# Optimization experiments

Measured on AMD Instinct MI355X. Metric: run time of the kernel, lower is better.

The kernel has to match this reference:

```python
import jax, jax.numpy as jnp
import numpy as np
from jax import lax

B, C, H, W = 1, 512, 64, 64
HEADS, GROUPS, STRIDE, KK = 8, 4, 2, 5
HC = C // HEADS          # 64 head channels
CG = C // GROUPS         # 128 group channels
GH = HEADS // GROUPS     # 2 heads per group
OFR = 2.0                # offset_range_factor
SCALE = HC ** -0.5


def ref_points(Hk, Wk):
    # torch linspace(0.5, Hk-0.5, Hk)/Hk*2-1 == (arange+0.5)/Hk*2-1
    ry = (jnp.arange(Hk, dtype=jnp.float32) + 0.5) / Hk * 2.0 - 1.0
    rx = (jnp.arange(Wk, dtype=jnp.float32) + 0.5) / Wk * 2.0 - 1.0
    return jnp.stack(jnp.meshgrid(ry, rx, indexing='ij'), axis=-1)  # [Hk,Wk,2] (y,x)


def _gather(img, ix, iy, Hi, Wi):
    # img [N,Cc,Hi,Wi]; ix,iy float index maps [N,...]; zero padding outside
    N, Cc = img.shape[0], img.shape[1]
    valid = ((ix >= 0) & (ix <= Wi - 1) & (iy >= 0) & (iy <= Hi - 1)).astype(img.dtype)
    ixc = jnp.clip(ix, 0, Wi - 1).astype(jnp.int32)
    iyc = jnp.clip(iy, 0, Hi - 1).astype(jnp.int32)
    idx = (iyc * Wi + ixc).reshape(N, -1)
    imgf = img.reshape(N, Cc, Hi * Wi)
    g = jax.vmap(lambda im, ii: im[:, ii])(imgf, idx).reshape((N, Cc) + ix.shape[1:])
    return g * valid[:, None]


def grid_sample(img, grid):
    # bilinear, align_corners=True, zeros padding; grid [...,(x,y)] in [-1,1]
    N, Cc, Hi, Wi = img.shape
    gx = (grid[..., 0] + 1.0) * 0.5 * (Wi - 1)
    gy = (grid[..., 1] + 1.0) * 0.5 * (Hi - 1)
    x0 = jnp.floor(gx); y0 = jnp.floor(gy)
    wx = gx - x0; wy = gy - y0
    w00 = ((1 - wx) * (1 - wy))[:, None]; w01 = (wx * (1 - wy))[:, None]
    w10 = ((1 - wx) * wy)[:, None]; w11 = (wx * wy)[:, None]
    return (_gather(img, x0, y0, Hi, Wi) * w00 + _gather(img, x0 + 1, y0, Hi, Wi) * w01
            + _gather(img, x0, y0 + 1, Hi, Wi) * w10 + _gather(img, x0 + 1, y0 + 1, Hi, Wi) * w11)


def conv1x1(w, b, x):  # x [B,C,H,W]
    return jnp.einsum('oc,bchw->bohw', w, x) + b[None, :, None, None]


def setup_inputs() -> dict:
    key = jax.random.key(0)
    ks = jax.random.split(key, 8)
    d = {}
    d['x'] = jax.random.normal(ks[0], (B, C, H, W), jnp.float32)
    d['wq'] = jax.random.normal(ks[1], (C, C), jnp.float32) * 0.04
    d['bq'] = jnp.zeros((C,), jnp.float32)
    d['wk'] = jax.random.normal(ks[2], (C, C), jnp.float32) * 0.04
    d['bk'] = jnp.zeros((C,), jnp.float32)
    d['wv'] = jax.random.normal(ks[3], (C, C), jnp.float32) * 0.04
    d['bv'] = jnp.zeros((C,), jnp.float32)
    d['wo'] = jax.random.normal(ks[4], (C, C), jnp.float32) * 0.04
    d['bo'] = jnp.zeros((C,), jnp.float32)
    d['w_off_dw'] = jax.random.normal(ks[5], (CG, 1, KK, KK), jnp.float32) * 0.1
    d['b_off_dw'] = jnp.zeros((CG,), jnp.float32)
    d['ln_g'] = jnp.ones((CG,), jnp.float32)
    d['ln_b'] = jnp.zeros((CG,), jnp.float32)
    d['w_off_pw'] = jax.random.normal(ks[6], (2, CG), jnp.float32) * 0.05
    d['rpe_table'] = jax.random.normal(ks[7], (HEADS, 2 * H - 1, 2 * W - 1), jnp.float32) * 0.01
    return d


def reference(x, wq, bq, wk, bk, wv, bv, wo, bo, w_off_dw, b_off_dw, ln_g, ln_b, w_off_pw, rpe_table):
    q = conv1x1(wq, bq, x)                                   # [B,C,H,W]
    q_off = q.reshape(B * GROUPS, CG, H, W)
    # conv_offset: depthwise 5x5 stride-2 -> LayerNorm(channels) -> GELU -> 1x1 to 2ch
    t = lax.conv_general_dilated(q_off, w_off_dw, (STRIDE, STRIDE),
                                 ((KK // 2, KK // 2), (KK // 2, KK // 2)),
                                 feature_group_count=CG,
                                 dimension_numbers=('NCHW', 'OIHW', 'NCHW'))
    t = t + b_off_dw[None, :, None, None]
    mu = t.mean(1, keepdims=True)
    var = ((t - mu) ** 2).mean(1, keepdims=True)
    t = (t - mu) * lax.rsqrt(var + 1e-5) * ln_g[None, :, None, None] + ln_b[None, :, None, None]
    t = jax.nn.gelu(t, approximate=False)
    offset = jnp.einsum('oc,bchw->bohw', w_off_pw, t)        # [B*G,2,Hk,Wk]
    Hk, Wk = offset.shape[2], offset.shape[3]
    ns = Hk * Wk
    orange = jnp.array([1.0 / Hk, 1.0 / Wk], dtype=x.dtype).reshape(1, 2, 1, 1)
    offset = jnp.tanh(offset) * orange * OFR
    offset = offset.transpose(0, 2, 3, 1)                    # [B*G,Hk,Wk,2] (y,x)
    ref = jnp.broadcast_to(ref_points(Hk, Wk)[None], (B * GROUPS, Hk, Wk, 2))
    pos = offset + ref
    xs = grid_sample(x.reshape(B * GROUPS, CG, H, W), pos[..., ::-1])  # [B*G,CG,Hk,Wk]
    xs = xs.reshape(B, C, ns)
    qf = q.reshape(B * HEADS, HC, H * W)
    k = (jnp.einsum('oc,bcn->bon', wk, xs) + bk[None, :, None]).reshape(B * HEADS, HC, ns)
    v = (jnp.einsum('oc,bcn->bon', wv, xs) + bv[None, :, None]).reshape(B * HEADS, HC, ns)
    attn = jnp.einsum('bcm,bcn->bmn', qf, k) * SCALE         # [B*heads, HW, ns]
    # relative position bias via grid_sample of the rpe table
    rpe = jnp.broadcast_to(rpe_table[None], (B, HEADS, 2 * H - 1, 2 * W - 1)).reshape(
        B * GROUPS, GH, 2 * H - 1, 2 * W - 1)
    qg = jnp.broadcast_to(ref_points(H, W).reshape(1, H * W, 2), (B * GROUPS, H * W, 2))
    disp = (qg[:, :, None, :] - pos.reshape(B * GROUPS, ns, 2)[:, None, :, :]) * 0.5
    bias = grid_sample(rpe, disp[..., ::-1]).reshape(B * HEADS, H * W, ns)
    attn = jax.nn.softmax(attn + bias, axis=2)
    out = jnp.einsum('bmn,bcn->bcm', attn, v).reshape(B, C, H, W)
    y = conv1x1(wo, bo, out)
    return (y, pos.reshape(B, GROUPS, Hk, Wk, 2), ref.reshape(B, GROUPS, Hk, Wk, 2))
```

## Files before the change

### kernel.cpp

```cpp
#include <hip/hip_runtime.h>
#include <hip/hip_fp16.h>
#include <math.h>

#define CC   512
#define HH   64
#define WW   64
#define HWN  4096
#define HEADS 8
#define GROUPS 4
#define HC   64
#define CG   128
#define NS   1024
#define HK   32
#define SCALE 0.125f
#define RPE_W 127
#define RPE_N 16129

typedef _Float16 f16x8 __attribute__((ext_vector_type(8)));
typedef float f32x4 __attribute__((ext_vector_type(4)));

__global__ __launch_bounds__(256) void gemm_bias_kernel(
    const float* __restrict__ A, const float* __restrict__ B,
    const float* __restrict__ bias, float* __restrict__ C,
    int N, int K)
{
  __shared__ __align__(16) float As[32][64];
  __shared__ __align__(16) float Bs[32][64];
  const int bn0 = blockIdx.x * 64;
  const int bm0 = blockIdx.y * 64;
  const int tid = threadIdx.x;
  const int tx = tid & 15, ty = tid >> 4;
  float acc[4][4] = {};

  const int am = tid >> 2;
  const int ak = (tid & 3) * 8;
  const int bn = tid & 63;
  const int bk = (tid >> 6) * 8;

  for (int kt = 0; kt < K; kt += 32) {
    float4 a0 = *(const float4*)&A[(size_t)(bm0 + am) * K + kt + ak];
    float4 a1 = *(const float4*)&A[(size_t)(bm0 + am) * K + kt + ak + 4];
    As[ak + 0][am] = a0.x; As[ak + 1][am] = a0.y;
    As[ak + 2][am] = a0.z; As[ak + 3][am] = a0.w;
    As[ak + 4][am] = a1.x; As[ak + 5][am] = a1.y;
    As[ak + 6][am] = a1.z; As[ak + 7][am] = a1.w;
    #pragma unroll
    for (int r = 0; r < 8; ++r)
      Bs[bk + r][bn] = B[(size_t)(kt + bk + r) * N + bn0 + bn];
    __syncthreads();
    #pragma unroll
    for (int kk = 0; kk < 32; ++kk) {
      float4 a = *(const float4*)&As[kk][ty * 4];
      float4 b = *(const float4*)&Bs[kk][tx * 4];
      acc[0][0] += a.x * b.x; acc[0][1] += a.x * b.y; acc[0][2] += a.x * b.z; acc[0][3] += a.x * b.w;
      acc[1][0] += a.y * b.x; acc[1][1] += a.y * b.y; acc[1][2] += a.y * b.z; acc[1][3] += a.y * b.w;
      acc[2][0] += a.z * b.x; acc[2][1] += a.z * b.y; acc[2][2] += a.z * b.z; acc[2][3] += a.z * b.w;
      acc[3][0] += a.w * b.x; acc[3][1] += a.w * b.y; acc[3][2] += a.w * b.z; acc[3][3] += a.w * b.w;
    }
    __syncthreads();
  }
  #pragma unroll
  for (int i = 0; i < 4; ++i) {
    float bi = bias[bm0 + ty * 4 + i];
    #pragma unroll
    for (int j = 0; j < 4; ++j)
      C[(size_t)(bm0 + ty * 4 + i) * N + bn0 + tx * 4 + j] = acc[i][j] + bi;
  }
}

__global__ __launch_bounds__(256) void dwconv_kernel(
    const float* __restrict__ q, const float* __restrict__ w_dw,
    const float* __restrict__ b_dw, float* __restrict__ t_ws)
{
  __shared__ __align__(16) float plane[HWN];
  const int c = blockIdx.x;
  const int g = blockIdx.y;
  const int tid = threadIdx.x;

  const float* qplane = q + (size_t)(g * CG + c) * HWN;
  for (int i = tid; i < HWN / 4; i += 256)
    ((float4*)plane)[i] = ((const float4*)qplane)[i];

  float wreg[25];
  #pragma unroll
  for (int t = 0; t < 25; ++t) wreg[t] = w_dw[c * 25 + t];
  const float bias = b_dw[c];

  __syncthreads();

  #pragma unroll
  for (int k = 0; k < 4; ++k) {
    int p = (k << 8) | tid;
    int oy = p >> 5, ox = p & 31;
    int iy0 = oy * 2 - 2, ix0 = ox * 2 - 2;
    float acc = bias;
    #pragma unroll
    for (int ky = 0; ky < 5; ++ky) {
      int iy = iy0 + ky;
      bool yok = (iy >= 0) & (iy <= 63);
      int iyc = min(max(iy, 0), 63);
      #pragma unroll
      for (int kx = 0; kx < 5; ++kx) {
        int ix = ix0 + kx;
        bool ok = yok & (ix >= 0) & (ix <= 63);
        int ixc = min(max(ix, 0), 63);
        float v = plane[iyc * 64 + ixc];
        acc += wreg[ky * 5 + kx] * (ok ? v : 0.f);
      }
    }
    t_ws[(size_t)(((g << 10) | p) << 7) + c] = acc;
  }
}

__device__ __forceinline__ float block_sum_128(float v, float* red, int c) {
  red[c] = v;
  __syncthreads();
  #pragma unroll
  for (int s = 64; s > 0; s >>= 1) {
    if (c < s) red[c] += red[c + s];
    __syncthreads();
  }
  float r = red[0];
  __syncthreads();
  return r;
}

__global__ __launch_bounds__(128) void lnpw_kernel(
    const float* __restrict__ t_ws,
    const float* __restrict__ ln_g, const float* __restrict__ ln_b,
    const float* __restrict__ w_pw,
    float* __restrict__ pos_ws, float* __restrict__ pos_out,
    float* __restrict__ ref_out)
{
  __shared__ float red[128];
  const int blk = blockIdx.x;
  const int g = blk >> 10, p = blk & 1023;
  const int oy = p >> 5, ox = p & 31;
  const int c = threadIdx.x;

  float t = t_ws[(size_t)blk * CG + c];
  float mu = block_sum_128(t, red, c) * (1.f / 128.f);
  float d = t - mu;
  float var = block_sum_128(d * d, red, c) * (1.f / 128.f);
  float u = d * rsqrtf(var + 1e-5f) * ln_g[c] + ln_b[c];
  float ge = 0.5f * u * (1.f + erff(u * 0.70710678118654752f));
  float sy = block_sum_128(w_pw[c] * ge, red, c);
  float sx = block_sum_128(w_pw[128 + c] * ge, red, c);
  if (c == 0) {
    const float scale = 2.0f / 32.0f;
    float offy = tanhf(sy) * scale;
    float offx = tanhf(sx) * scale;
    float refy = ((float)oy + 0.5f) * (2.f / 32.f) - 1.f;
    float refx = ((float)ox + 0.5f) * (2.f / 32.f) - 1.f;
    float py = offy + refy, px = offx + refx;
    int o = (g << 10) | p;
    pos_ws[o * 2 + 0] = py;  pos_ws[o * 2 + 1] = px;
    pos_out[o * 2 + 0] = py; pos_out[o * 2 + 1] = px;
    ref_out[o * 2 + 0] = refy; ref_out[o * 2 + 1] = refx;
  }
}

__device__ __forceinline__ float tap_img(const float* __restrict__ img,
                                         float xf, float yf, float lim, int Wr) {
  bool v = (xf >= 0.f) & (xf <= lim) & (yf >= 0.f) & (yf <= lim);
  float xc = fminf(fmaxf(xf, 0.f), lim);
  float yc = fminf(fmaxf(yf, 0.f), lim);
  int ix = (int)xc, iy = (int)yc;
  float val = img[iy * Wr + ix];
  return v ? val : 0.f;
}

__global__ __launch_bounds__(256) void sample_kernel(
    const float* __restrict__ x, const float* __restrict__ pos_ws,
    float* __restrict__ xs)
{
  int t = blockIdx.x * 256 + threadIdx.x;
  int c = t >> 10;
  int p = t & 1023;
  int g = c >> 7;
  float py = pos_ws[((g << 10) | p) * 2 + 0];
  float px = pos_ws[((g << 10) | p) * 2 + 1];
  float gx = (px + 1.f) * 0.5f * 63.f;
  float gy = (py + 1.f) * 0.5f * 63.f;
  float x0 = floorf(gx), y0 = floorf(gy);
  float wx = gx - x0, wy = gy - y0;
  const float* img = x + (size_t)c * HWN;
  float v00 = tap_img(img, x0,       y0,       63.f, 64);
  float v01 = tap_img(img, x0 + 1.f, y0,       63.f, 64);
  float v10 = tap_img(img, x0,       y0 + 1.f, 63.f, 64);
  float v11 = tap_img(img, x0 + 1.f, y0 + 1.f, 63.f, 64);
  xs[(size_t)c * NS + p] =
      (v00 * (1.f - wx) + v01 * wx) * (1.f - wy) +
      (v10 * (1.f - wx) + v11 * wx) * wy;
}

__device__ __forceinline__ void split_f16(float x, ushort& h, ushort& l) {
  __half xh = __float2half(x);
  float hf = __half2float(xh);
  __half xl = __float2half(x - hf);
  h = __half_as_ushort(xh);
  l = __half_as_ushort(xl);
}

__global__ __launch_bounds__(256) void tsplit_kernel(
    const float* __restrict__ src, ushort* __restrict__ dh,
    ushort* __restrict__ dl, int ncols)
{
  __shared__ float tile[64][65];
  const int ct = blockIdx.x, hh = blockIdx.y;
  const int tid = threadIdx.x;
  for (int i = tid; i < 4096; i += 256) {
    int ch = i >> 6, m = i & 63;
    tile[ch][m] = src[(size_t)(hh * 64 + ch) * ncols + ct * 64 + m];
  }
  __syncthreads();
  for (int i = tid; i < 4096; i += 256) {
    int m = i >> 6, ch = i & 63;
    ushort h, l;
    split_f16(tile[ch][m], h, l);
    size_t o = ((size_t)hh * ncols + ct * 64 + m) * 64 + ch;
    dh[o] = h; dl[o] = l;
  }
}

__global__ __launch_bounds__(256) void vsplit_kernel(
    const float* __restrict__ src, ushort* __restrict__ dh,
    ushort* __restrict__ dl)
{
  int i = blockIdx.x * 256 + threadIdx.x;
  ushort h, l;
  split_f16(src[i], h, l);
  dh[i] = h; dl[i] = l;
}

__global__ __launch_bounds__(256) void attn_kernel(
    const float*  __restrict__ qb,
    const ushort* __restrict__ kth, const ushort* __restrict__ ktl,
    const ushort* __restrict__ vhb, const ushort* __restrict__ vlb,
    const float* __restrict__ pos,
    const float* __restrict__ rpe,
    float* __restrict__ ob)
{
  __shared__ __align__(16) uint ps32[4][16][64];
  __shared__ float olds[4][64][17];

  const int h = blockIdx.y, m0 = blockIdx.x * 64, g = h >> 1;
  const int tid = threadIdx.x;
  const int w = tid >> 6, lane = tid & 63, l15 = lane & 15, lq = lane >> 4;
  const float* rpeh = rpe + h * RPE_N;

  const int mg = m0 + w * 16 + l15;
  f16x8 qfh[2], qfl[2];
  #pragma unroll
  for (int kst = 0; kst < 2; ++kst) {
    union { f16x8 v; ushort u[8]; } Hh, Ll;
    #pragma unroll
    for (int j = 0; j < 8; ++j) {
      int ch = kst * 32 + lq * 8 + j;
      float qv = qb[((size_t)(h * 64 + ch)) * 4096 + mg];
      ushort hh, ll;
      split_f16(qv, hh, ll);
      Hh.u[j] = hh; Ll.u[j] = ll;
    }
    qfh[kst] = Hh.v; qfl[kst] = Ll.v;
  }

  const float qgy = ((float)(m0 >> 6) + 0.5f) * (2.f / 64.f) - 1.f;
  const float ayp = qgy * 31.5f + 63.f;
  float axp[4];
  #pragma unroll
  for (int r = 0; r < 4; ++r) {
    int ml = w * 16 + lq * 4 + r;
    float qgx = ((float)ml + 0.5f) * (2.f / 64.f) - 1.f;
    axp[r] = qgx * 31.5f + 63.f;
  }

  float mrun[4], lrun[4];
  f32x4 O[4];
  #pragma unroll
  for (int r = 0; r < 4; ++r) { mrun[r] = -INFINITY; lrun[r] = 0.f; }
  #pragma unroll
  for (int t = 0; t < 4; ++t) O[t] = (f32x4)0.f;

  for (int c = 0; c < 16; ++c) {
    const int n0c = c * 64;

    f16x8 kfh[4][2], kfl[4][2];
    #pragma unroll
    for (int nt = 0; nt < 4; ++nt) {
      const ushort* b0 = kth + ((size_t)h * 1024 + n0c + nt * 16 + l15) * 64 + lq * 8;
      const ushort* b1 = ktl + ((size_t)h * 1024 + n0c + nt * 16 + l15) * 64 + lq * 8;
      kfh[nt][0] = *(const f16x8*)(b0);  kfh[nt][1] = *(const f16x8*)(b0 + 32);
      kfl[nt][0] = *(const f16x8*)(b1);  kfl[nt][1] = *(const f16x8*)(b1 + 32);
    }

    f32x4 s[4];
    #pragma unroll
    for (int nt = 0; nt < 4; ++nt) {
      f32x4 acc = (f32x4)0.f;
      acc = __builtin_amdgcn_mfma_f32_16x16x32_f16(qfh[0], kfh[nt][0], acc, 0, 0, 0);
      acc = __builtin_amdgcn_mfma_f32_16x16x32_f16(qfh[0], kfl[nt][0], acc, 0, 0, 0);
      acc = __builtin_amdgcn_mfma_f32_16x16x32_f16(qfl[0], kfh[nt][0], acc, 0, 0, 0);
      acc = __builtin_amdgcn_mfma_f32_16x16x32_f16(qfh[1], kfh[nt][1], acc, 0, 0, 0);
      acc = __builtin_amdgcn_mfma_f32_16x16x32_f16(qfh[1], kfl[nt][1], acc, 0, 0, 0);
      acc = __builtin_amdgcn_mfma_f32_16x16x32_f16(qfl[1], kfh[nt][1], acc, 0, 0, 0);
      s[nt] = acc;
    }

    f16x8 vfh[4][2], vfl[4][2];
    #pragma unroll
    for (int ct = 0; ct < 4; ++ct) {
      const ushort* b0 = vhb + ((size_t)(h * 64 + ct * 16 + l15)) * 1024 + n0c + lq * 8;
      const ushort* b1 = vlb + ((size_t)(h * 64 + ct * 16 + l15)) * 1024 + n0c + lq * 8;
      vfh[ct][0] = *(const f16x8*)(b0);  vfh[ct][1] = *(const f16x8*)(b0 + 32);
      vfl[ct][0] = *(const f16x8*)(b1);  vfl[ct][1] = *(const f16x8*)(b1 + 32);
    }

    #pragma unroll
    for (int nt = 0; nt < 4; ++nt) {
      int n = n0c + nt * 16 + l15;
      float py = pos[((g << 10) | n) * 2 + 0];
      float px = pos[((g << 10) | n) * 2 + 1];
      float bx = px * 31.5f;
      float gy = ayp - py * 31.5f;
      float y0f = floorf(gy);
      float wy1 = gy - y0f, wy0 = 1.f - wy1;
      bool yv0 = (y0f >= 0.f) & (y0f <= 126.f);
      bool yv1 = (y0f >= -1.f) & (y0f <= 125.f);
      int rr0 = (int)fminf(fmaxf(y0f, 0.f), 126.f) * RPE_W;
      int rr1 = (int)fminf(fmaxf(y0f + 1.f, 0.f), 126.f) * RPE_W;
      #pragma unroll
      for (int r = 0; r < 4; ++r) {
        float gx = axp[r] - bx;
        float x0f = floorf(gx);
        float wx = gx - x0f;
        bool xv0 = (x0f >= 0.f) & (x0f <= 126.f);
        bool xv1 = (x0f >= -1.f) & (x0f <= 125.f);
        int xi0 = (int)fminf(fmaxf(x0f, 0.f), 126.f);
        int xi1 = (int)fminf(fmaxf(x0f + 1.f, 0.f), 126.f);
        float t00 = rpeh[rr0 + xi0];
        float t01 = rpeh[rr0 + xi1];
        float t10 = rpeh[rr1 + xi0];
        float t11 = rpeh[rr1 + xi1];
        float v00 = (xv0 & yv0) ? t00 : 0.f;
        float v01 = (xv1 & yv0) ? t01 : 0.f;
        float v10 = (xv0 & yv1) ? t10 : 0.f;
        float v11 = (xv1 & yv1) ? t11 : 0.f;
        float bt = v00 * (1.f - wx) + v01 * wx;
        float bb = v10 * (1.f - wx) + v11 * wx;
        s[nt][r] = s[nt][r] * SCALE + bt * wy0 + bb * wy1;
      }
    }

    #pragma unroll
    for (int r = 0; r < 4; ++r) {
      float rm = fmaxf(fmaxf(s[0][r], s[1][r]), fmaxf(s[2][r], s[3][r]));
      rm = fmaxf(rm, __shfl_xor(rm, 1, 16));
      rm = fmaxf(rm, __shfl_xor(rm, 2, 16));
      rm = fmaxf(rm, __shfl_xor(rm, 4, 16));
      rm = fmaxf(rm, __shfl_xor(rm, 8, 16));
      float mnew = fmaxf(mrun[r], rm);
      float alpha = __expf(mrun[r] - mnew);
      mrun[r] = mnew;
      float rs = 0.f;
      #pragma unroll
      for (int nt = 0; nt < 4; ++nt) {
        float p = __expf(s[nt][r] - mnew);
        s[nt][r] = p;
        rs += p;
      }
      rs += __shfl_xor(rs, 1, 16);
      rs += __shfl_xor(rs, 2, 16);
      rs += __shfl_xor(rs, 4, 16);
      rs += __shfl_xor(rs, 8, 16);
      lrun[r] = lrun[r] * alpha + rs;
      #pragma unroll
      for (int ct = 0; ct < 4; ++ct) O[ct][r] *= alpha;
    }

    #pragma unroll
    for (int nt = 0; nt < 4; ++nt) {
      #pragma unroll
      for (int r = 0; r < 4; ++r) {
        ushort hh, ll;
        split_f16(s[nt][r], hh, ll);
        uint packed = (uint)hh | ((uint)ll << 16);
        int m = lq * 4 + r;
        int n = nt * 16 + l15;
        ps32[w][m][(n & 3) | ((((n >> 2) ^ m) & 15) << 2)] = packed;
      }
    }

    f16x8 pfh[2], pfl[2];
    #pragma unroll
    for (int nst = 0; nst < 2; ++nst) {
      int s0 = nst * 8 + lq * 2;
      uint4 u0 = *(const uint4*)&ps32[w][l15][((s0 ^ l15) & 15) << 2];
      uint4 u1 = *(const uint4*)&ps32[w][l15][(((s0 + 1) ^ l15) & 15) << 2];
      union { f16x8 v; ushort u[8]; } ah, al;
      uint t0[8] = {u0.x, u0.y, u0.z, u0.w, u1.x, u1.y, u1.z, u1.w};
      #pragma unroll
      for (int j = 0; j < 8; ++j) {
        ah.u[j] = (ushort)(t0[j] & 0xffffu);
        al.u[j] = (ushort)(t0[j] >> 16);
      }
      pfh[nst] = ah.v;
      pfl[nst] = al.v;
    }

    #pragma unroll
    for (int ct = 0; ct < 4; ++ct) {
      f32x4 acc = O[ct];
      acc = __builtin_amdgcn_mfma_f32_16x16x32_f16(pfh[0], vfh[ct][0], acc, 0, 0, 0);
      acc = __builtin_amdgcn_mfma_f32_16x16x32_f16(pfh[0], vfl[ct][0], acc, 0, 0, 0);
      acc = __builtin_amdgcn_mfma_f32_16x16x32_f16(pfl[0], vfh[ct][0], acc, 0, 0, 0);
      acc = __builtin_amdgcn_mfma_f32_16x16x32_f16(pfh[1], vfh[ct][1], acc, 0, 0, 0);
      acc = __builtin_amdgcn_mfma_f32_16x16x32_f16(pfh[1], vfl[ct][1], acc, 0, 0, 0);
      acc = __builtin_amdgcn_mfma_f32_16x16x32_f16(pfl[1], vfh[ct][1], acc, 0, 0, 0);
      O[ct] = acc;
    }
  }

  float inv[4];
  #pragma unroll
  for (int r = 0; r < 4; ++r) inv[r] = 1.f / lrun[r];
  #pragma unroll
  for (int ct = 0; ct < 4; ++ct)
    #pragma unroll
    for (int r = 0; r < 4; ++r)
      olds[w][ct * 16 + l15][lq * 4 + r] = O[ct][r] * inv[r];

  #pragma unroll
  for (int it = 0; it < 16; ++it) {
    int ch = it * 4 + lq;
    ob[((size_t)(h * 64 + ch)) * 4096 + m0 + w * 16 + l15] = olds[w][ch][l15];
  }
}

extern "C" void kernel_launch(void* const* d_in, const int* in_sizes, int n_in,
                              void* d_out, int out_size, void* d_ws, size_t ws_size,
                              hipStream_t stream) {
  const float* x     = (const float*)d_in[0];
  const float* wq    = (const float*)d_in[1];
  const float* bq    = (const float*)d_in[2];
  const float* wk    = (const float*)d_in[3];
  const float* bk    = (const float*)d_in[4];
  const float* wv    = (const float*)d_in[5];
  const float* bv    = (const float*)d_in[6];
  const float* wo    = (const float*)d_in[7];
  const float* bo    = (const float*)d_in[8];
  const float* w_dw  = (const float*)d_in[9];
  const float* b_dw  = (const float*)d_in[10];
  const float* ln_g  = (const float*)d_in[11];
  const float* ln_b  = (const float*)d_in[12];
  const float* w_pw  = (const float*)d_in[13];
  const float* rpe   = (const float*)d_in[14];

  float* out = (float*)d_out;
  float* y_out   = out;
  float* pos_out = out + 2097152;
  float* ref_out = out + 2097152 + 8192;

  float* ws = (float*)d_ws;
  float* qbuf  = ws;
  float* posws = qbuf + 2097152;
  float* xsbuf = posws + 8192;
  float* kbuf  = xsbuf + 524288;
  float* vbuf  = kbuf + 524288;
  float* obuf  = vbuf + 524288;
  float* t_ws  = xsbuf;
  ushort* kth = (ushort*)xsbuf;
  ushort* ktl = kth + 524288;
  ushort* vhb = (ushort*)kbuf;
  ushort* vlb = vhb + 524288;

  gemm_bias_kernel<<<dim3(HWN / 64, CC / 64), 256, 0, stream>>>(wq, x, bq, qbuf, HWN, CC);
  dwconv_kernel<<<dim3(CG, GROUPS), 256, 0, stream>>>(qbuf, w_dw, b_dw, t_ws);
  lnpw_kernel<<<dim3(GROUPS * NS), 128, 0, stream>>>(t_ws, ln_g, ln_b, w_pw,
                                                     posws, pos_out, ref_out);
  sample_kernel<<<dim3(CC * NS / 256), 256, 0, stream>>>(x, posws, xsbuf);
  gemm_bias_kernel<<<dim3(NS / 64, CC / 64), 256, 0, stream>>>(wk, xsbuf, bk, kbuf, NS, CC);
  gemm_bias_kernel<<<dim3(NS / 64, CC / 64), 256, 0, stream>>>(wv, xsbuf, bv, vbuf, NS, CC);
  tsplit_kernel<<<dim3(NS / 64, HEADS), 256, 0, stream>>>(kbuf, kth, ktl, NS);
  vsplit_kernel<<<dim3(CC * NS / 256), 256, 0, stream>>>(vbuf, vhb, vlb);
  attn_kernel<<<dim3(HWN / 64, HEADS), 256, 0, stream>>>(qbuf, kth, ktl,
                                                         vhb, vlb, posws, rpe, obuf);
  gemm_bias_kernel<<<dim3(HWN / 64, CC / 64), 256, 0, stream>>>(wo, obuf, bo, y_out, HWN, CC);
}
```

Measured before the change: 415.1 us.

## Use split-fp16 MFMA GEMMs for projections and prefetch K in attention

The four 1x1 projection GEMMs (q, k, v, out) move from the fp32 gemm_bias_kernel to a new MFMA kernel. Each runs on fp16 hi/lo split operands, using transpose-split passes for activations and split passes for weights. It is gated on the workspace being large enough. The attention kernel double-buffers K fragments and position loads for the next chunk and computes the rpe bias before the QK MFMAs, with a 2-waves-per-SIMD launch bound. This adds several extra split and transpose launches each call and more register pressure in attention, in exchange for matrix-core throughput.

```diff
diff --git a/kernel.cpp b/kernel.cpp
--- a/kernel.cpp
+++ b/kernel.cpp
@@ -223,6 +223,27 @@
   }
 }
 
+__global__ __launch_bounds__(256) void tsplitg_kernel(
+    const float* __restrict__ src, ushort* __restrict__ dh,
+    ushort* __restrict__ dl, int R, int N)
+{
+  __shared__ float tile[64][65];
+  const int c0 = blockIdx.x * 64, r0 = blockIdx.y * 64;
+  const int tid = threadIdx.x;
+  for (int i = tid; i < 4096; i += 256) {
+    int rr = i >> 6, cc = i & 63;
+    tile[rr][cc] = src[(size_t)(r0 + rr) * N + c0 + cc];
+  }
+  __syncthreads();
+  for (int i = tid; i < 4096; i += 256) {
+    int cc = i >> 6, rr = i & 63;
+    ushort h, l;
+    split_f16(tile[rr][cc], h, l);
+    size_t o = (size_t)(c0 + cc) * R + r0 + rr;
+    dh[o] = h; dl[o] = l;
+  }
+}
+
 __global__ __launch_bounds__(256) void vsplit_kernel(
     const float* __restrict__ src, ushort* __restrict__ dh,
     ushort* __restrict__ dl)
@@ -233,7 +254,73 @@
   dh[i] = h; dl[i] = l;
 }
 
-__global__ __launch_bounds__(256) void attn_kernel(
+__global__ __launch_bounds__(256, 2) void mfma_gemm_kernel(
+    const ushort* __restrict__ Ah, const ushort* __restrict__ Al,
+    const ushort* __restrict__ Bth, const ushort* __restrict__ Btl,
+    const float* __restrict__ bias, float* __restrict__ C,
+    int N, int K)
+{
+  const int bn0 = blockIdx.x * 64, bm0 = blockIdx.y * 64;
+  const int tid = threadIdx.x, lane = tid & 63;
+  const int w = tid >> 6, l15 = lane & 15, lq = lane >> 4;
+  const size_t arow = (size_t)(bm0 + w * 16 + l15) * K;
+  const int KS = K >> 5;
+
+  f32x4 acc[4];
+  #pragma unroll
+  for (int nt = 0; nt < 4; ++nt) acc[nt] = (f32x4)0.f;
+
+  f16x8 aHa, aLa, aHb, aLb;
+  f16x8 bHa[4], bLa[4], bHb[4], bLb[4];
+
+  aHa = *(const f16x8*)(Ah + arow + lq * 8);
+  aLa = *(const f16x8*)(Al + arow + lq * 8);
+  #pragma unroll
+  for (int nt = 0; nt < 4; ++nt) {
+    size_t br = (size_t)(bn0 + nt * 16 + l15) * K + lq * 8;
+    bHa[nt] = *(const f16x8*)(Bth + br);
+    bLa[nt] = *(const f16x8*)(Btl + br);
+  }
+
+  auto bodyG = [&](int ks, f16x8& ach, f16x8& acl, f16x8 (&bch)[4], f16x8 (&bcl)[4],
+                   f16x8& anh, f16x8& anl, f16x8 (&bnh)[4], f16x8 (&bnl)[4]) {
+    int kn = (ks + 1 < KS) ? ks + 1 : ks;
+    int ko = kn * 32 + lq * 8;
+    anh = *(const f16x8*)(Ah + arow + ko);
+    anl = *(const f16x8*)(Al + arow + ko);
+    #pragma unroll
+    for (int nt = 0; nt < 4; ++nt) {
+      size_t br = (size_t)(bn0 + nt * 16 + l15) * K + ko;
+      bnh[nt] = *(const f16x8*)(Bth + br);
+      bnl[nt] = *(const f16x8*)(Btl + br);
+    }
+    #pragma unroll
+    for (int nt = 0; nt < 4; ++nt) {
+      f32x4 a = acc[nt];
+      a = __builtin_amdgcn_mfma_f32_16x16x32_f16(ach, bch[nt], a, 0, 0, 0);
+      a = __builtin_amdgcn_mfma_f32_16x16x32_f16(ach, bcl[nt], a, 0, 0, 0);
+      a = __builtin_amdgcn_mfma_f32_16x16x32_f16(acl, bch[nt], a, 0, 0, 0);
+      acc[nt] = a;
+    }
+  };
+
+  for (int ks = 0; ks < KS; ks += 2) {
+    bodyG(ks,     aHa, aLa, bHa, bLa, aHb, aLb, bHb, bLb);
+    bodyG(ks + 1, aHb, aLb, bHb, bLb, aHa, aLa, bHa, bLa);
+  }
+
+  float bv[4];
+  #pragma unroll
+  for (int r = 0; r < 4; ++r) bv[r] = bias[bm0 + w * 16 + lq * 4 + r];
+  #pragma unroll
+  for (int nt = 0; nt < 4; ++nt)
+    #pragma unroll
+    for (int r = 0; r < 4; ++r)
+      C[(size_t)(bm0 + w * 16 + lq * 4 + r) * N + bn0 + nt * 16 + l15] =
+          acc[nt][r] + bv[r];
+}
+
+__global__ __launch_bounds__(256, 2) void attn_kernel(
     const float*  __restrict__ qb,
     const ushort* __restrict__ kth, const ushort* __restrict__ ktl,
     const ushort* __restrict__ vhb, const ushort* __restrict__ vlb,
@@ -282,47 +369,42 @@
   #pragma unroll
   for (int t = 0; t < 4; ++t) O[t] = (f32x4)0.f;
 
-  for (int c = 0; c < 16; ++c) {
+  float pyv[4], pxv[4];
+  #pragma unroll
+  for (int nt = 0; nt < 4; ++nt) {
+    int n = nt * 16 + l15;
+    pyv[nt] = pos[((g << 10) | n) * 2 + 0];
+    pxv[nt] = pos[((g << 10) | n) * 2 + 1];
+  }
+
+  f16x8 kAh[4][2], kAl[4][2], kBh[4][2], kBl[4][2];
+  #pragma unroll
+  for (int nt = 0; nt < 4; ++nt) {
+    const ushort* b0 = kth + ((size_t)h * 1024 + nt * 16 + l15) * 64 + lq * 8;
+    const ushort* b1 = ktl + ((size_t)h * 1024 + nt * 16 + l15) * 64 + lq * 8;
+    kAh[nt][0] = *(const f16x8*)b0;  kAh[nt][1] = *(const f16x8*)(b0 + 32);
+    kAl[nt][0] = *(const f16x8*)b1;  kAl[nt][1] = *(const f16x8*)(b1 + 32);
+  }
+
+  auto body = [&](int c, f16x8 (&kch)[4][2], f16x8 (&kcl)[4][2],
+                  f16x8 (&knh)[4][2], f16x8 (&knl)[4][2]) {
     const int n0c = c * 64;
-
-    f16x8 kfh[4][2], kfl[4][2];
+    const int cn = (c < 15) ? c + 1 : 15;
+    const int n0n = cn * 64;
+
     #pragma unroll
     for (int nt = 0; nt < 4; ++nt) {
-      const ushort* b0 = kth + ((size_t)h * 1024 + n0c + nt * 16 + l15) * 64 + lq * 8;
-      const ushort* b1 = ktl + ((size_t)h * 1024 + n0c + nt * 16 + l15) * 64 + lq * 8;
-      kfh[nt][0] = *(const f16x8*)(b0);  kfh[nt][1] = *(const f16x8*)(b0 + 32);
-      kfl[nt][0] = *(const f16x8*)(b1);  kfl[nt][1] = *(const f16x8*)(b1 + 32);
-    }
-
-    f32x4 s[4];
+      const ushort* b0 = kth + ((size_t)h * 1024 + n0n + nt * 16 + l15) * 64 + lq * 8;
+      const ushort* b1 = ktl + ((size_t)h * 1024 + n0n + nt * 16 + l15) * 64 + lq * 8;
+      knh[nt][0] = *(const f16x8*)b0;  knh[nt][1] = *(const f16x8*)(b0 + 32);
+      knl[nt][0] = *(const f16x8*)b1;  knl[nt][1] = *(const f16x8*)(b1 + 32);
+    }
+
+    float bias[4][4];
     #pragma unroll
     for (int nt = 0; nt < 4; ++nt) {
-      f32x4 acc = (f32x4)0.f;
-      acc = __builtin_amdgcn_mfma_f32_16x16x32_f16(qfh[0], kfh[nt][0], acc, 0, 0, 0);
-      acc = __builtin_amdgcn_mfma_f32_16x16x32_f16(qfh[0], kfl[nt][0], acc, 0, 0, 0);
-      acc = __builtin_amdgcn_mfma_f32_16x16x32_f16(qfl[0], kfh[nt][0], acc, 0, 0, 0);
-      acc = __builtin_amdgcn_mfma_f32_16x16x32_f16(qfh[1], kfh[nt][1], acc, 0, 0, 0);
-      acc = __builtin_amdgcn_mfma_f32_16x16x32_f16(qfh[1], kfl[nt][1], acc, 0, 0, 0);
-      acc = __builtin_amdgcn_mfma_f32_16x16x32_f16(qfl[1], kfh[nt][1], acc, 0, 0, 0);
-      s[nt] = acc;
-    }
-
-    f16x8 vfh[4][2], vfl[4][2];
-    #pragma unroll
-    for (int ct = 0; ct < 4; ++ct) {
-      const ushort* b0 = vhb + ((size_t)(h * 64 + ct * 16 + l15)) * 1024 + n0c + lq * 8;
-      const ushort* b1 = vlb + ((size_t)(h * 64 + ct * 16 + l15)) * 1024 + n0c + lq * 8;
-      vfh[ct][0] = *(const f16x8*)(b0);  vfh[ct][1] = *(const f16x8*)(b0 + 32);
-      vfl[ct][0] = *(const f16x8*)(b1);  vfl[ct][1] = *(const f16x8*)(b1 + 32);
-    }
-
-    #pragma unroll
-    for (int nt = 0; nt < 4; ++nt) {
-      int n = n0c + nt * 16 + l15;
-      float py = pos[((g << 10) | n) * 2 + 0];
-      float px = pos[((g << 10) | n) * 2 + 1];
-      float bx = px * 31.5f;
-      float gy = ayp - py * 31.5f;
+      float bx = pxv[nt] * 31.5f;
+      float gy = ayp - pyv[nt] * 31.5f;
       float y0f = floorf(gy);
       float wy1 = gy - y0f, wy0 = 1.f - wy1;
       bool yv0 = (y0f >= 0.f) & (y0f <= 126.f);
@@ -348,8 +430,42 @@
         float v11 = (xv1 & yv1) ? t11 : 0.f;
         float bt = v00 * (1.f - wx) + v01 * wx;
         float bb = v10 * (1.f - wx) + v11 * wx;
-        s[nt][r] = s[nt][r] * SCALE + bt * wy0 + bb * wy1;
+        bias[nt][r] = bt * wy0 + bb * wy1;
       }
+    }
+
+    f32x4 s[4];
+    #pragma unroll
+    for (int nt = 0; nt < 4; ++nt) {
+      f32x4 acc = (f32x4)0.f;
+      acc = __builtin_amdgcn_mfma_f32_16x16x32_f16(qfh[0], kch[nt][0], acc, 0, 0, 0);
+      acc = __builtin_amdgcn_mfma_f32_16x16x32_f16(qfh[0], kcl[nt][0], acc, 0, 0, 0);
+      acc = __builtin_amdgcn_mfma_f32_16x16x32_f16(qfl[0], kch[nt][0], acc, 0, 0, 0);
+      acc = __builtin_amdgcn_mfma_f32_16x16x32_f16(qfh[1], kch[nt][1], acc, 0, 0, 0);
+      acc = __builtin_amdgcn_mfma_f32_16x16x32_f16(qfh[1], kcl[nt][1], acc, 0, 0, 0);
+      acc = __builtin_amdgcn_mfma_f32_16x16x32_f16(qfl[1], kch[nt][1], acc, 0, 0, 0);
+      s[nt] = acc;
+    }
+
+    #pragma unroll
+    for (int nt = 0; nt < 4; ++nt)
+      #pragma unroll
+      for (int r = 0; r < 4; ++r)
+        s[nt][r] = s[nt][r] * SCALE + bias[nt][r];
+
+    f16x8 vfh[4][2], vfl[4][2];
+    #pragma unroll
+    for (int ct = 0; ct < 4; ++ct) {
+      const ushort* b0 = vhb + ((size_t)(h * 64 + ct * 16 + l15)) * 1024 + n0c + lq * 8;
+      const ushort* b1 = vlb + ((size_t)(h * 64 + ct * 16 + l15)) * 1024 + n0c + lq * 8;
+      vfh[ct][0] = *(const f16x8*)b0;  vfh[ct][1] = *(const f16x8*)(b0 + 32);
+      vfl[ct][0] = *(const f16x8*)b1;  vfl[ct][1] = *(const f16x8*)(b1 + 32);
+    }
+    #pragma unroll
+    for (int nt = 0; nt < 4; ++nt) {
+      int n = n0n + nt * 16 + l15;
+      pyv[nt] = pos[((g << 10) | n) * 2 + 0];
+      pxv[nt] = pos[((g << 10) | n) * 2 + 1];
     }
 
     #pragma unroll
@@ -390,7 +506,6 @@
         ps32[w][m][(n & 3) | ((((n >> 2) ^ m) & 15) << 2)] = packed;
       }
     }
-
     f16x8 pfh[2], pfl[2];
     #pragma unroll
     for (int nst = 0; nst < 2; ++nst) {
@@ -419,6 +534,11 @@
       acc = __builtin_amdgcn_mfma_f32_16x16x32_f16(pfl[1], vfh[ct][1], acc, 0, 0, 0);
       O[ct] = acc;
     }
+  };
+
+  for (int c = 0; c < 16; c += 2) {
+    body(c,     kAh, kAl, kBh, kBl);
+    body(c + 1, kBh, kBl, kAh, kAl);
   }
 
   float inv[4];
@@ -474,16 +594,55 @@
   ushort* vhb = (ushort*)kbuf;
   ushort* vlb = vhb + 524288;
 
-  gemm_bias_kernel<<<dim3(HWN / 64, CC / 64), 256, 0, stream>>>(wq, x, bq, qbuf, HWN, CC);
+  float* wsp = obuf + 2097152;
+  const size_t need = (size_t)(6823936) * 4;
+  const bool use_mfma_gemm = (ws_size >= need);
+
+  ushort* wqh = (ushort*)wsp;
+  ushort* wql = wqh + 262144;
+  ushort* wkh = wql + 262144;
+  ushort* wkl = wkh + 262144;
+  ushort* wvh = wkl + 262144;
+  ushort* wvl = wvh + 262144;
+  ushort* woh = wvl + 262144;
+  ushort* wol = woh + 262144;
+  ushort* xTh  = (ushort*)obuf;
+  ushort* xTl  = xTh + 2097152;
+  ushort* xsTh = (ushort*)obuf;
+  ushort* xsTl = xsTh + 524288;
+  ushort* oTh  = (ushort*)qbuf;
+  ushort* oTl  = oTh + 2097152;
+
+  if (use_mfma_gemm) {
+    vsplit_kernel<<<1024, 256, 0, stream>>>(wq, wqh, wql);
+    vsplit_kernel<<<1024, 256, 0, stream>>>(wk, wkh, wkl);
+    vsplit_kernel<<<1024, 256, 0, stream>>>(wv, wvh, wvl);
+    vsplit_kernel<<<1024, 256, 0, stream>>>(wo, woh, wol);
+    tsplitg_kernel<<<dim3(64, 8), 256, 0, stream>>>(x, xTh, xTl, 512, 4096);
+    mfma_gemm_kernel<<<dim3(64, 8), 256, 0, stream>>>(wqh, wql, xTh, xTl, bq, qbuf, 4096, 512);
+  } else {
+    gemm_bias_kernel<<<dim3(HWN / 64, CC / 64), 256, 0, stream>>>(wq, x, bq, qbuf, HWN, CC);
+  }
   dwconv_kernel<<<dim3(CG, GROUPS), 256, 0, stream>>>(qbuf, w_dw, b_dw, t_ws);
   lnpw_kernel<<<dim3(GROUPS * NS), 128, 0, stream>>>(t_ws, ln_g, ln_b, w_pw,
                                                      posws, pos_out, ref_out);
   sample_kernel<<<dim3(CC * NS / 256), 256, 0, stream>>>(x, posws, xsbuf);
-  gemm_bias_kernel<<<dim3(NS / 64, CC / 64), 256, 0, stream>>>(wk, xsbuf, bk, kbuf, NS, CC);
-  gemm_bias_kernel<<<dim3(NS / 64, CC / 64), 256, 0, stream>>>(wv, xsbuf, bv, vbuf, NS, CC);
+  if (use_mfma_gemm) {
+    tsplitg_kernel<<<dim3(16, 8), 256, 0, stream>>>(xsbuf, xsTh, xsTl, 512, 1024);
+    mfma_gemm_kernel<<<dim3(16, 8), 256, 0, stream>>>(wkh, wkl, xsTh, xsTl, bk, kbuf, 1024, 512);
+    mfma_gemm_kernel<<<dim3(16, 8), 256, 0, stream>>>(wvh, wvl, xsTh, xsTl, bv, vbuf, 1024, 512);
+  } else {
+    gemm_bias_kernel<<<dim3(NS / 64, CC / 64), 256, 0, stream>>>(wk, xsbuf, bk, kbuf, NS, CC);
+    gemm_bias_kernel<<<dim3(NS / 64, CC / 64), 256, 0, stream>>>(wv, xsbuf, bv, vbuf, NS, CC);
+  }
   tsplit_kernel<<<dim3(NS / 64, HEADS), 256, 0, stream>>>(kbuf, kth, ktl, NS);
   vsplit_kernel<<<dim3(CC * NS / 256), 256, 0, stream>>>(vbuf, vhb, vlb);
   attn_kernel<<<dim3(HWN / 64, HEADS), 256, 0, stream>>>(qbuf, kth, ktl,
                                                          vhb, vlb, posws, rpe, obuf);
-  gemm_bias_kernel<<<dim3(HWN / 64, CC / 64), 256, 0, stream>>>(wo, obuf, bo, y_out, HWN, CC);
-}
+  if (use_mfma_gemm) {
+    tsplitg_kernel<<<dim3(64, 8), 256, 0, stream>>>(obuf, oTh, oTl, 512, 4096);
+    mfma_gemm_kernel<<<dim3(64, 8), 256, 0, stream>>>(woh, wol, oTh, oTl, bo, y_out, 4096, 512);
+  } else {
+    gemm_bias_kernel<<<dim3(HWN / 64, CC / 64), 256, 0, stream>>>(wo, obuf, bo, y_out, HWN, CC);
+  }
+}
```

Result: slower. 457.6 us (+10.2%).

## Split attention KV range across two blocks and merge with combine kernel

Applied to the files above, without the earlier changes.

Adds a flash-decoding style split of the key/value sequence into two halves, launching twice as many attention blocks that each write unnormalized partial outputs plus running max and sum. A new combine kernel rescales and merges the two partials. This raises the number of attention workgroups from 512 to 1024 to better fill the GPU, at the cost of extra global traffic for the partials and an additional launch. The split path is taken only if the workspace is large enough, otherwise the original single-pass path is used.

```diff
diff --git a/kernel.cpp b/kernel.cpp
--- a/kernel.cpp
+++ b/kernel.cpp
@@ -239,15 +239,21 @@
     const ushort* __restrict__ vhb, const ushort* __restrict__ vlb,
     const float* __restrict__ pos,
     const float* __restrict__ rpe,
-    float* __restrict__ ob)
+    float* __restrict__ oO,
+    float* __restrict__ mlm,
+    float* __restrict__ mll,
+    int cps, int mode)
 {
   __shared__ __align__(16) uint ps32[4][16][64];
   __shared__ float olds[4][64][17];
 
   const int h = blockIdx.y, m0 = blockIdx.x * 64, g = h >> 1;
+  const int sp = blockIdx.z;
+  const int c0 = sp * cps, c1 = c0 + cps;
   const int tid = threadIdx.x;
   const int w = tid >> 6, lane = tid & 63, l15 = lane & 15, lq = lane >> 4;
   const float* rpeh = rpe + h * RPE_N;
+  float* oOs = oO + (size_t)sp * 2097152;
 
   const int mg = m0 + w * 16 + l15;
   f16x8 qfh[2], qfl[2];
@@ -282,7 +288,7 @@
   #pragma unroll
   for (int t = 0; t < 4; ++t) O[t] = (f32x4)0.f;
 
-  for (int c = 0; c < 16; ++c) {
+  for (int c = c0; c < c1; ++c) {
     const int n0c = c * 64;
 
     f16x8 kfh[4][2], kfl[4][2];
@@ -390,7 +396,6 @@
         ps32[w][m][(n & 3) | ((((n >> 2) ^ m) & 15) << 2)] = packed;
       }
     }
-
     f16x8 pfh[2], pfl[2];
     #pragma unroll
     for (int nst = 0; nst < 2; ++nst) {
@@ -421,20 +426,71 @@
     }
   }
 
-  float inv[4];
-  #pragma unroll
-  for (int r = 0; r < 4; ++r) inv[r] = 1.f / lrun[r];
-  #pragma unroll
-  for (int ct = 0; ct < 4; ++ct)
-    #pragma unroll
-    for (int r = 0; r < 4; ++r)
-      olds[w][ct * 16 + l15][lq * 4 + r] = O[ct][r] * inv[r];
-
+  if (mode == 0) {
+    float inv[4];
+    #pragma unroll
+    for (int r = 0; r < 4; ++r) inv[r] = 1.f / lrun[r];
+    #pragma unroll
+    for (int ct = 0; ct < 4; ++ct)
+      #pragma unroll
+      for (int r = 0; r < 4; ++r)
+        olds[w][ct * 16 + l15][lq * 4 + r] = O[ct][r] * inv[r];
+  } else {
+    #pragma unroll
+    for (int ct = 0; ct < 4; ++ct)
+      #pragma unroll
+      for (int r = 0; r < 4; ++r)
+        olds[w][ct * 16 + l15][lq * 4 + r] = O[ct][r];
+    if (l15 == 0) {
+      float* mm = mlm + (size_t)sp * 32768 + h * 4096;
+      float* ll = mll + (size_t)sp * 32768 + h * 4096;
+      #pragma unroll
+      for (int r = 0; r < 4; ++r) {
+        int row = m0 + w * 16 + lq * 4 + r;
+        mm[row] = mrun[r];
+        ll[row] = lrun[r];
+      }
+    }
+  }
   #pragma unroll
   for (int it = 0; it < 16; ++it) {
     int ch = it * 4 + lq;
-    ob[((size_t)(h * 64 + ch)) * 4096 + m0 + w * 16 + l15] = olds[w][ch][l15];
-  }
+    oOs[((size_t)(h * 64 + ch)) * 4096 + m0 + w * 16 + l15] = olds[w][ch][l15];
+  }
+}
+
+__global__ __launch_bounds__(256) void combine_kernel(
+    float* __restrict__ part,
+    const float* __restrict__ mlm,
+    const float* __restrict__ mll)
+{
+  int idx = blockIdx.x * 256 + threadIdx.x;
+  int ch = idx >> 10, f4m = idx & 1023;
+  int h = ch >> 6;
+  float4 p0 = ((const float4*)part)[idx];
+  float4 p1 = ((const float4*)(part + 2097152))[idx];
+  float4 m0 = *(const float4*)&mlm[h * 4096 + f4m * 4];
+  float4 m1 = *(const float4*)&mlm[32768 + h * 4096 + f4m * 4];
+  float4 l0 = *(const float4*)&mll[h * 4096 + f4m * 4];
+  float4 l1 = *(const float4*)&mll[32768 + h * 4096 + f4m * 4];
+  float4 r;
+  {
+    float M = fmaxf(m0.x, m1.x), e0 = __expf(m0.x - M), e1 = __expf(m1.x - M);
+    r.x = (p0.x * e0 + p1.x * e1) / (l0.x * e0 + l1.x * e1);
+  }
+  {
+    float M = fmaxf(m0.y, m1.y), e0 = __expf(m0.y - M), e1 = __expf(m1.y - M);
+    r.y = (p0.y * e0 + p1.y * e1) / (l0.y * e0 + l1.y * e1);
+  }
+  {
+    float M = fmaxf(m0.z, m1.z), e0 = __expf(m0.z - M), e1 = __expf(m1.z - M);
+    r.z = (p0.z * e0 + p1.z * e1) / (l0.z * e0 + l1.z * e1);
+  }
+  {
+    float M = fmaxf(m0.w, m1.w), e0 = __expf(m0.w - M), e1 = __expf(m1.w - M);
+    r.w = (p0.w * e0 + p1.w * e1) / (l0.w * e0 + l1.w * e1);
+  }
+  ((float4*)part)[idx] = r;
 }
 
 extern "C" void kernel_launch(void* const* d_in, const int* in_sizes, int n_in,
@@ -468,11 +524,17 @@
   float* kbuf  = xsbuf + 524288;
   float* vbuf  = kbuf + 524288;
   float* obuf  = vbuf + 524288;
+  float* part1 = obuf + 2097152;
+  float* mlm   = part1 + 2097152;
+  float* mll   = mlm + 65536;
   float* t_ws  = xsbuf;
   ushort* kth = (ushort*)xsbuf;
   ushort* ktl = kth + 524288;
   ushort* vhb = (ushort*)kbuf;
   ushort* vlb = vhb + 524288;
+
+  const size_t need_split = (size_t)(mll + 65536 - ws) * sizeof(float);
+  const bool use_split = (ws_size >= need_split);
 
   gemm_bias_kernel<<<dim3(HWN / 64, CC / 64), 256, 0, stream>>>(wq, x, bq, qbuf, HWN, CC);
   dwconv_kernel<<<dim3(CG, GROUPS), 256, 0, stream>>>(qbuf, w_dw, b_dw, t_ws);
@@ -483,7 +545,13 @@
   gemm_bias_kernel<<<dim3(NS / 64, CC / 64), 256, 0, stream>>>(wv, xsbuf, bv, vbuf, NS, CC);
   tsplit_kernel<<<dim3(NS / 64, HEADS), 256, 0, stream>>>(kbuf, kth, ktl, NS);
   vsplit_kernel<<<dim3(CC * NS / 256), 256, 0, stream>>>(vbuf, vhb, vlb);
-  attn_kernel<<<dim3(HWN / 64, HEADS), 256, 0, stream>>>(qbuf, kth, ktl,
-                                                         vhb, vlb, posws, rpe, obuf);
+  if (use_split) {
+    attn_kernel<<<dim3(HWN / 64, HEADS, 2), 256, 0, stream>>>(
+        qbuf, kth, ktl, vhb, vlb, posws, rpe, obuf, mlm, mll, 8, 1);
+    combine_kernel<<<2048, 256, 0, stream>>>(obuf, mlm, mll);
+  } else {
+    attn_kernel<<<dim3(HWN / 64, HEADS, 1), 256, 0, stream>>>(
+        qbuf, kth, ktl, vhb, vlb, posws, rpe, obuf, mlm, mll, 16, 0);
+  }
   gemm_bias_kernel<<<dim3(HWN / 64, CC / 64), 256, 0, stream>>>(wo, obuf, bo, y_out, HWN, CC);
 }
```

Result: no change. 421.8 us (+1.6%).
